# Kernel tuning notes

Measured on AMD Instinct MI355X. Metric: run time of the kernel, lower is better.

## Reference

```python
import jax, jax.numpy as jnp
import numpy as np

N = 15000        # nodes
E = 240000       # edges (avg degree 16)
IN_DIM = 100
HID = 128
N_ETYPES = 13
N_STEPS = 6
N_GRAPHS = 64
N_CLASSES = 10


def setup_inputs() -> dict:
    key = jax.random.key(0)
    ks = jax.random.split(key, 12)
    feat = jax.random.normal(ks[0], (N, IN_DIM), dtype=jnp.float32)
    src = jax.random.randint(ks[1], (E,), 0, N, dtype=jnp.int32)
    dst = jax.random.randint(ks[2], (E,), 0, N, dtype=jnp.int32)
    etypes = jax.random.randint(ks[3], (E,), 0, N_ETYPES, dtype=jnp.int32)
    graph_ids = jnp.sort(jax.random.randint(ks[4], (N,), 0, N_GRAPHS, dtype=jnp.int32))
    s = 1.0 / np.sqrt(HID)
    W_e = jax.random.normal(ks[5], (N_ETYPES, HID, HID), dtype=jnp.float32) * s
    b_e = jax.random.normal(ks[6], (N_ETYPES, HID), dtype=jnp.float32) * s
    W_ih = jax.random.normal(ks[7], (3 * HID, HID), dtype=jnp.float32) * s
    W_hh = jax.random.normal(ks[8], (3 * HID, HID), dtype=jnp.float32) * s
    b_ih = jax.random.normal(ks[9], (3 * HID,), dtype=jnp.float32) * s
    b_hh = jax.random.normal(ks[10], (3 * HID,), dtype=jnp.float32) * s
    W_cls = jax.random.normal(ks[11], (N_CLASSES, HID), dtype=jnp.float32) * s
    b_cls = jnp.zeros((N_CLASSES,), dtype=jnp.float32)
    return {"feat": feat, "src": src, "dst": dst, "etypes": etypes,
            "graph_ids": graph_ids, "W_e": W_e, "b_e": b_e,
            "W_ih": W_ih, "W_hh": W_hh, "b_ih": b_ih, "b_hh": b_hh,
            "W_cls": W_cls, "b_cls": b_cls}


def _ggnn_forward(feat, src, dst, etypes, graph_ids, W_e, b_e, W_ih, W_hh, b_ih, b_hh, W_cls, b_cls):
    # DGL GatedGraphConv: zero-pad input features up to out_feats
    h = jnp.pad(feat, ((0, 0), (0, HID - IN_DIM)))  # [N, HID]
    for _ in range(N_STEPS):
        # per-etype linear transform of all nodes: [T, N, HID]
        Wh = jnp.einsum('nd,tdh->tnh', h, W_e) + b_e[:, None, :]
        # per-edge message = linear[etype](h[src]) via gather; scatter-sum to dst
        msg = Wh[etypes, src]                                  # [E, HID]
        a = jax.ops.segment_sum(msg, dst, num_segments=N)      # [N, HID]
        # torch GRUCell update (gate order r, z, n)
        gi = a @ W_ih.T + b_ih
        gh = h @ W_hh.T + b_hh
        ir, iz, inn = jnp.split(gi, 3, axis=-1)
        hr, hz, hn = jnp.split(gh, 3, axis=-1)
        r = jax.nn.sigmoid(ir + hr)
        z = jax.nn.sigmoid(iz + hz)
        n = jnp.tanh(inn + r * hn)
        h = (1.0 - z) * n + z * h
    # dgl.sum_nodes: sum node states per graph in the batch
    hg = jax.ops.segment_sum(h, graph_ids, num_segments=N_GRAPHS)  # [G, HID]
    return hg @ W_cls.T + b_cls                                    # [G, N_CLASSES]


def reference(feat, src, dst, etypes, graph_ids, W_e, b_e, W_ih, W_hh, b_ih, b_hh, W_cls, b_cls):
    return _ggnn_forward(feat, src, dst, etypes, graph_ids, W_e, b_e, W_ih, W_hh, b_ih, b_hh, W_cls, b_cls)
```

## Files before the change

### kernel.cpp

```cpp
#include <hip/hip_runtime.h>
#include <math.h>

#define N_NODES 15000
#define NPAD    15104
#define E_EDGES 240000
#define IN_DIM  100
#define HID     128
#define N_ETYPES 13
#define N_STEPS  6
#define N_GRAPHS 64
#define N_CLASSES 10
#define NTS     (N_ETYPES * NPAD)
#define NSB     384

typedef short v8bf __attribute__((ext_vector_type(8)));
typedef float v4f  __attribute__((ext_vector_type(4)));

union FragU { uint4 u; v8bf b; };

static __device__ __forceinline__ float bf2f(unsigned short u) {
    union { unsigned int i; float f; } x; x.i = ((unsigned int)u) << 16; return x.f;
}
static __device__ __forceinline__ unsigned short f2bf(float f) {
    union { float f; unsigned int i; } x; x.f = f;
    unsigned int u = x.i;
    u = (u + 0x7fff + ((u >> 16) & 1)) >> 16;
    return (unsigned short)u;
}
static __device__ __forceinline__ float sigm(float x) { return 1.f / (1.f + expf(-x)); }

__global__ __launch_bounds__(256) void k_initW(
    const float* __restrict__ feat,
    const float* __restrict__ W_e, const float* __restrict__ W_ih, const float* __restrict__ W_hh,
    float* __restrict__ h32, unsigned short* __restrict__ h_hi, unsigned short* __restrict__ h_lo,
    unsigned short* __restrict__ WeH,
    unsigned short* __restrict__ WihH, unsigned short* __restrict__ WhhH)
{
    int idx = blockIdx.x * 256 + threadIdx.x;
    const int IH = NPAD * HID;
    const int NE = N_ETYPES * 2048;
    const int NG = 16 * 384;
    if (idx < IH) {
        int n = idx >> 7, c = idx & 127;
        float v = 0.f;
        if (n < N_NODES && c < IN_DIM) v = feat[n * IN_DIM + c];
        h32[idx] = v;
        unsigned short hi = f2bf(v);
        h_hi[idx] = hi;
        h_lo[idx] = f2bf(v - bf2f(hi));
        return;
    }
    int f = idx - IH;
    unsigned short th[8];
    if (f < NE) {
        int t = f >> 11, r = f & 2047, kcsub = r >> 7, c = r & 127;
        #pragma unroll
        for (int j = 0; j < 8; ++j)
            th[j] = f2bf(W_e[(long)t * 16384 + (kcsub * 8 + j) * 128 + c]);
        *(uint4*)(WeH + (long)t * 16384 + ((kcsub << 7) + c) * 8) = *(uint4*)th;
    } else if (f < NE + 2 * NG) {
        int f2 = f - NE;
        const float* srcp = (f2 < NG) ? W_ih : W_hh;
        unsigned short* dh = (f2 < NG) ? WihH : WhhH;
        int g = (f2 < NG) ? f2 : f2 - NG;
        int kcsub = g / 384, c = g - kcsub * 384;
        #pragma unroll
        for (int j = 0; j < 8; ++j)
            th[j] = f2bf(srcp[(long)c * 128 + kcsub * 8 + j]);
        *(uint4*)(dh + ((long)kcsub * 384 + c) * 8) = *(uint4*)th;
    }
}

__global__ __launch_bounds__(256) void k_zero2(int* __restrict__ deg, int* __restrict__ used) {
    int idx = blockIdx.x * 256 + threadIdx.x;
    if (idx < NPAD) deg[idx] = 0;
    else if (idx < NPAD + NTS) used[idx - NPAD] = 0;
}

__global__ __launch_bounds__(256) void k_count_mark(const int* __restrict__ src,
                                                    const int* __restrict__ dst,
                                                    const int* __restrict__ et,
                                                    int* __restrict__ deg,
                                                    int* __restrict__ used) {
    int e = blockIdx.x * 256 + threadIdx.x;
    if (e >= E_EDGES) return;
    atomicAdd(&deg[dst[e]], 1);
    used[et[e] * NPAD + src[e]] = 1;
}

__global__ __launch_bounds__(1024) void k_scan(const int* __restrict__ deg,
                                               int* __restrict__ rowptr, int* __restrict__ cursor) {
    __shared__ int part[1024];
    int tid = threadIdx.x;
    const int CH = 15;
    int base = tid * CH;
    int local[CH]; int s = 0;
    #pragma unroll
    for (int i = 0; i < CH; ++i) {
        int d = (base + i < NPAD) ? deg[base + i] : 0;
        local[i] = s; s += d;
    }
    part[tid] = s; __syncthreads();
    for (int off = 1; off < 1024; off <<= 1) {
        int v = (tid >= off) ? part[tid - off] : 0;
        __syncthreads();
        part[tid] += v;
        __syncthreads();
    }
    int excl = (tid > 0) ? part[tid - 1] : 0;
    #pragma unroll
    for (int i = 0; i < CH; ++i)
        if (base + i < NPAD) { rowptr[base + i] = excl + local[i]; cursor[base + i] = excl + local[i]; }
    if (tid == 0) rowptr[NPAD] = part[1023];
}

__global__ __launch_bounds__(512) void k_su1(const int* __restrict__ used, int* __restrict__ bsum) {
    __shared__ int sh[512];
    int tid = threadIdx.x;
    int i = blockIdx.x * 512 + tid;
    sh[tid] = (i < NTS) ? used[i] : 0;
    __syncthreads();
    for (int off = 256; off > 0; off >>= 1) {
        if (tid < off) sh[tid] += sh[tid + off];
        __syncthreads();
    }
    if (tid == 0) bsum[blockIdx.x] = sh[0];
}

__global__ __launch_bounds__(512) void k_su2(const int* __restrict__ bsum, int* __restrict__ bofs) {
    __shared__ int sh[512];
    int tid = threadIdx.x;
    int v = (tid < NSB) ? bsum[tid] : 0;
    sh[tid] = v; __syncthreads();
    for (int off = 1; off < 512; off <<= 1) {
        int u = (tid >= off) ? sh[tid - off] : 0;
        __syncthreads();
        sh[tid] += u;
        __syncthreads();
    }
    if (tid < NSB) bofs[tid] = sh[tid] - v;
}

__global__ __launch_bounds__(512) void k_su3(const int* __restrict__ used,
                                             const int* __restrict__ bofs,
                                             int* __restrict__ slot,
                                             int* __restrict__ rowlist,
                                             int* __restrict__ tbase) {
    __shared__ int sh[512];
    int tid = threadIdx.x;
    int i = blockIdx.x * 512 + tid;
    int f = (i < NTS) ? used[i] : 0;
    sh[tid] = f; __syncthreads();
    for (int off = 1; off < 512; off <<= 1) {
        int u = (tid >= off) ? sh[tid - off] : 0;
        __syncthreads();
        sh[tid] += u;
        __syncthreads();
    }
    int g = bofs[blockIdx.x] + sh[tid] - f;
    if (i <= NTS) {
        if (i < NTS) slot[i] = g;
        int t = i / NPAD;
        if (i - t * NPAD == 0 || i == NTS) tbase[t] = g;
        if (f) rowlist[g] = i - t * NPAD;
    }
}

__global__ __launch_bounds__(256) void k_fill(const int* __restrict__ src, const int* __restrict__ dst,
                                              const int* __restrict__ et, const int* __restrict__ slot,
                                              int* __restrict__ cursor, int* __restrict__ eidx) {
    int e = blockIdx.x * 256 + threadIdx.x;
    if (e >= E_EDGES) return;
    int d = dst[e];
    int pos = atomicAdd(&cursor[d], 1);
    eidx[pos] = slot[et[e] * NPAD + src[e]];
}

__global__ __launch_bounds__(512) void k_egemm(
    const unsigned short* __restrict__ Ahi, const unsigned short* __restrict__ Alo,
    const uint4* __restrict__ BH,
    const float* __restrict__ bias, const int* __restrict__ tbase,
    const int* __restrict__ rowlist, unsigned short* __restrict__ C)
{
    __shared__ uint4 blds[2048];
    const int NW = 118 * N_ETYPES;
    const int q = NW / 8, r8 = NW % 8;
    int bid = blockIdx.x;
    int xcd = bid & 7, ii = bid >> 3;
    int lid = (xcd < r8 ? xcd * (q + 1) : r8 * (q + 1) + (xcd - r8) * q) + ii;
    int rg = lid / N_ETYPES, t = lid - rg * N_ETYPES;

    int base = tbase[t], end = tbase[t + 1];
    if (rg * 128 >= end - base) return;

    int tid = threadIdx.x;
    {
        const uint4* bh = BH + t * 2048;
        #pragma unroll
        for (int it = 0; it < 4; ++it) {
            int f = it * 512 + tid;
            blds[f] = bh[f];
        }
    }
    __syncthreads();

    int lane = tid & 63, w = tid >> 6;
    int gs0 = base + rg * 128 + w * 16;
    int l15 = lane & 15, lsub = lane >> 4;

    int rowslot = gs0 + l15;
    int srcrow = (rowslot < end) ? rowlist[rowslot] : 0;

    FragU ah[4], al[4];
    const char* Ahb = (const char*)Ahi;
    const char* Alb = (const char*)Alo;
    #pragma unroll
    for (int kc = 0; kc < 4; ++kc) {
        long boff = (long)srcrow * 256 + kc * 64 + lsub * 16;
        ah[kc].u = *(const uint4*)(Ahb + boff);
        al[kc].u = *(const uint4*)(Alb + boff);
    }

    v4f acc[8];
    #pragma unroll
    for (int c8 = 0; c8 < 8; ++c8) acc[c8] = (v4f)(0.f);

    #pragma unroll
    for (int kc = 0; kc < 4; ++kc)
        #pragma unroll
        for (int c8 = 0; c8 < 8; ++c8) {
            int bi = (kc * 4 + lsub) * 128 + c8 * 16 + l15;
            FragU bhf; bhf.u = blds[bi];
            acc[c8] = __builtin_amdgcn_mfma_f32_16x16x32_bf16(ah[kc].b, bhf.b, acc[c8], 0, 0, 0);
            acc[c8] = __builtin_amdgcn_mfma_f32_16x16x32_bf16(al[kc].b, bhf.b, acc[c8], 0, 0, 0);
        }

    const float* bs = bias + t * 128;
    int gbase = gs0 + lsub * 4;
    #pragma unroll
    for (int c8 = 0; c8 < 8; ++c8) {
        int col = c8 * 16 + l15;
        float bv = bs[col];
        #pragma unroll
        for (int i = 0; i < 4; ++i) {
            int gs2 = gbase + i;
            if (gs2 < end) C[(long)gs2 * 128 + col] = f2bf(acc[c8][i] + bv);
        }
    }
}

__global__ __launch_bounds__(256) void k_agg(
    const int* __restrict__ rowptr, const int* __restrict__ eidx,
    const uint4* __restrict__ Wh,
    uint4* __restrict__ a_hi)
{
    int d = blockIdx.x * 4 + (threadIdx.x >> 6);
    int lane = threadIdx.x & 63;
    int g = lane >> 4, c16 = lane & 15;
    int s = rowptr[d], e = rowptr[d + 1];
    float acc[8] = {};
    for (int i = s + g; i < e; i += 4) {
        int slot = eidx[i];
        uint4 v = Wh[(long)slot * 16 + c16];
        unsigned int ua[4] = {v.x, v.y, v.z, v.w};
        #pragma unroll
        for (int q = 0; q < 4; ++q) {
            acc[2 * q]     += bf2f((unsigned short)(ua[q] & 0xffff));
            acc[2 * q + 1] += bf2f((unsigned short)(ua[q] >> 16));
        }
    }
    #pragma unroll
    for (int q = 0; q < 8; ++q) {
        acc[q] += __shfl_xor(acc[q], 16);
        acc[q] += __shfl_xor(acc[q], 32);
    }
    if (g == 0) {
        unsigned short hb[8];
        #pragma unroll
        for (int q = 0; q < 8; ++q) hb[q] = f2bf(acc[q]);
        a_hi[(long)d * 16 + c16] = *(uint4*)hb;
    }
}

__global__ __launch_bounds__(512) void k_gru(
    const unsigned short* __restrict__ a_hi,
    const uint4* __restrict__ WihH, const uint4* __restrict__ WhhH,
    const float* __restrict__ b_ih, const float* __restrict__ b_hh,
    float* __restrict__ h32,
    unsigned short* __restrict__ h_hi, unsigned short* __restrict__ h_lo)
{
    int tid = threadIdx.x, lane = tid & 63, cg = tid >> 6;
    int r0 = blockIdx.x * 16;
    int l15 = lane & 15, lsub = lane >> 4;

    FragU aa[4], hh[2][4];
    {
        const char* ahb = (const char*)a_hi;
        const char* hhb = (const char*)h_hi;
        const char* hlb = (const char*)h_lo;
        #pragma unroll
        for (int kc = 0; kc < 4; ++kc) {
            long boff = (long)(r0 + l15) * 256 + kc * 64 + lsub * 16;
            aa[kc].u    = *(const uint4*)(ahb + boff);
            hh[0][kc].u = *(const uint4*)(hhb + boff);
            hh[1][kc].u = *(const uint4*)(hlb + boff);
        }
    }
    __syncthreads();

    v4f accI[3], accH[3];
    #pragma unroll
    for (int g = 0; g < 3; ++g) { accI[g] = (v4f)(0.f); accH[g] = (v4f)(0.f); }

    #pragma unroll
    for (int kc = 0; kc < 4; ++kc)
        #pragma unroll
        for (int g = 0; g < 3; ++g) {
            int bi = (kc * 4 + lsub) * 384 + g * 128 + cg * 16 + l15;
            FragU wih, whh;
            wih.u = WihH[bi]; whh.u = WhhH[bi];
            accI[g] = __builtin_amdgcn_mfma_f32_16x16x32_bf16(aa[kc].b,    wih.b, accI[g], 0, 0, 0);
            accH[g] = __builtin_amdgcn_mfma_f32_16x16x32_bf16(hh[0][kc].b, whh.b, accH[g], 0, 0, 0);
            accH[g] = __builtin_amdgcn_mfma_f32_16x16x32_bf16(hh[1][kc].b, whh.b, accH[g], 0, 0, 0);
        }

    int c = cg * 16 + l15;
    float bir = b_ih[c], biz = b_ih[c + 128], bin = b_ih[c + 256];
    float bhr = b_hh[c], bhz = b_hh[c + 128], bhn = b_hh[c + 256];
    #pragma unroll
    for (int i = 0; i < 4; ++i) {
        int row = r0 + lsub * 4 + i;
        float ir = accI[0][i] + bir, iz = accI[1][i] + biz, inn = accI[2][i] + bin;
        float hr = accH[0][i] + bhr, hz = accH[1][i] + bhz, hn = accH[2][i] + bhn;
        float rr = sigm(ir + hr);
        float zg = sigm(iz + hz);
        float ng = tanhf(inn + rr * hn);
        long off = (long)row * 128 + c;
        float ho = h32[off];
        float hv = (1.f - zg) * ng + zg * ho;
        if (row < N_NODES) {
            h32[off] = hv;
            unsigned short hi_ = f2bf(hv);
            h_hi[off] = hi_;
            h_lo[off] = f2bf(hv - bf2f(hi_));
        }
    }
}

__global__ __launch_bounds__(256) void k_pool(const float* __restrict__ h32,
                                              const int* __restrict__ gid,
                                              float* __restrict__ hg) {
    int idx = blockIdx.x * 256 + threadIdx.x;
    if (idx >= N_NODES * HID) return;
    int n = idx >> 7, c = idx & 127;
    atomicAdd(&hg[gid[n] * HID + c], h32[idx]);
}

__global__ __launch_bounds__(256) void k_zero(float* __restrict__ p, long n4) {
    long i = (long)blockIdx.x * 256 + threadIdx.x;
    if (i < n4) ((float4*)p)[i] = make_float4(0.f, 0.f, 0.f, 0.f);
}

__global__ __launch_bounds__(640) void k_cls(const float* __restrict__ hg,
                                             const float* __restrict__ Wc,
                                             const float* __restrict__ bc,
                                             float* __restrict__ out) {
    int tid = threadIdx.x;
    if (tid >= N_GRAPHS * N_CLASSES) return;
    int g = tid / N_CLASSES, c = tid - g * N_CLASSES;
    float s = bc[c];
    for (int k = 0; k < HID; ++k) s = fmaf(hg[g * HID + k], Wc[c * HID + k], s);
    out[tid] = s;
}

extern "C" void kernel_launch(void* const* d_in, const int* in_sizes, int n_in,
                              void* d_out, int out_size, void* d_ws, size_t ws_size,
                              hipStream_t stream) {
    const float* feat  = (const float*)d_in[0];
    const int*   src   = (const int*)d_in[1];
    const int*   dst   = (const int*)d_in[2];
    const int*   et    = (const int*)d_in[3];
    const int*   gid   = (const int*)d_in[4];
    const float* W_e   = (const float*)d_in[5];
    const float* b_e   = (const float*)d_in[6];
    const float* W_ih  = (const float*)d_in[7];
    const float* W_hh  = (const float*)d_in[8];
    const float* b_ih  = (const float*)d_in[9];
    const float* b_hh  = (const float*)d_in[10];
    const float* W_cls = (const float*)d_in[11];
    const float* b_cls = (const float*)d_in[12];
    float* out = (float*)d_out;

    char* p = (char*)d_ws;
    auto alloc = [&](size_t bytes) { char* r = p; p += (bytes + 255) & ~(size_t)255; return r; };
    float*          h32  = (float*)alloc((size_t)NPAD * 128 * 4);
    unsigned short* h_hi = (unsigned short*)alloc((size_t)NPAD * 128 * 2);
    unsigned short* h_lo = (unsigned short*)alloc((size_t)NPAD * 128 * 2);
    unsigned short* a_hi = (unsigned short*)alloc((size_t)NPAD * 128 * 2);
    unsigned short* Wh   = (unsigned short*)alloc((size_t)NTS * 128 * 2);
    unsigned short* WeH  = (unsigned short*)alloc((size_t)N_ETYPES * 16384 * 2);
    unsigned short* WihH = (unsigned short*)alloc((size_t)16 * 384 * 8 * 2);
    unsigned short* WhhH = (unsigned short*)alloc((size_t)16 * 384 * 8 * 2);
    int* deg     = (int*)alloc((size_t)NPAD * 4);
    int* rowptr  = (int*)alloc((size_t)(NPAD + 1) * 4);
    int* cursor  = (int*)alloc((size_t)NPAD * 4);
    int* eidx    = (int*)alloc((size_t)E_EDGES * 4);
    int* used    = (int*)alloc((size_t)NTS * 4);
    int* slot    = (int*)alloc((size_t)NTS * 4);
    int* rowlist = (int*)alloc((size_t)NTS * 4);
    int* bsum    = (int*)alloc((size_t)NSB * 4);
    int* bofs    = (int*)alloc((size_t)NSB * 4);
    int* tbase   = (int*)alloc((size_t)(N_ETYPES + 1) * 4);
    float* hg    = (float*)alloc((size_t)N_GRAPHS * HID * 4);

    const int IW_GRID = (NPAD * HID + N_ETYPES * 2048 + 2 * 16 * 384 + 255) / 256;
    k_initW<<<IW_GRID, 256, 0, stream>>>(feat, W_e, W_ih, W_hh, h32, h_hi, h_lo,
                                         WeH, WihH, WhhH);
    k_zero2<<<(NPAD + NTS + 255) / 256, 256, 0, stream>>>(deg, used);
    k_count_mark<<<(E_EDGES + 255) / 256, 256, 0, stream>>>(src, dst, et, deg, used);
    k_scan<<<1, 1024, 0, stream>>>(deg, rowptr, cursor);
    k_su1<<<NSB, 512, 0, stream>>>(used, bsum);
    k_su2<<<1, 512, 0, stream>>>(bsum, bofs);
    k_su3<<<NSB, 512, 0, stream>>>(used, bofs, slot, rowlist, tbase);
    k_fill<<<(E_EDGES + 255) / 256, 256, 0, stream>>>(src, dst, et, slot, cursor, eidx);

    for (int step = 0; step < N_STEPS; ++step) {
        k_egemm<<<118 * N_ETYPES, 512, 0, stream>>>(
            h_hi, h_lo, (const uint4*)WeH, b_e, tbase, rowlist, Wh);
        k_agg<<<NPAD / 4, 256, 0, stream>>>(rowptr, eidx, (const uint4*)Wh, (uint4*)a_hi);
        k_gru<<<NPAD / 16, 512, 0, stream>>>(
            a_hi, (const uint4*)WihH, (const uint4*)WhhH,
            b_ih, b_hh, h32, h_hi, h_lo);
    }

    k_zero<<<(N_GRAPHS * HID / 4 + 255) / 256, 256, 0, stream>>>(hg, N_GRAPHS * HID / 4);
    k_pool<<<(N_NODES * HID + 255) / 256, 256, 0, stream>>>(h32, gid, hg);
    k_cls<<<1, 640, 0, stream>>>(hg, W_cls, b_cls, out);
}
```

Baseline: 505.1 us.

## Aggregate source states per (dst, etype) before transform and fuse into one kernel

Replaces transform-then-gather-scatter with gather-then-transform. Edges are bucketed by (dst, etype) via a CSR. Each wave sums the fp32 source states per etype and multiplies the sum by W_e with split-bf16 MFMA, while the bias is precomputed as count times b_e per node. This removes the large per-(etype, node) Wh intermediate and its write/read traffic. In exchange each block rereads h rows for every edge, loops serially over 13 etypes with per-lane edge loops, and runs only 236 blocks. Each block also loads W_e directly from global memory instead of staging it in LDS.

```diff
diff --git a/kernel.cpp b/kernel.cpp
--- a/kernel.cpp
+++ b/kernel.cpp
@@ -71,54 +71,24 @@
     }
 }
 
-__global__ __launch_bounds__(256) void k_zero2(int* __restrict__ deg, int* __restrict__ used) {
+__global__ __launch_bounds__(256) void k_zeroi(int* __restrict__ p, int n) {
     int idx = blockIdx.x * 256 + threadIdx.x;
-    if (idx < NPAD) deg[idx] = 0;
-    else if (idx < NPAD + NTS) used[idx - NPAD] = 0;
-}
-
-__global__ __launch_bounds__(256) void k_count_mark(const int* __restrict__ src,
-                                                    const int* __restrict__ dst,
-                                                    const int* __restrict__ et,
-                                                    int* __restrict__ deg,
-                                                    int* __restrict__ used) {
+    if (idx < n) p[idx] = 0;
+}
+
+__global__ __launch_bounds__(256) void k_countDT(const int* __restrict__ dst,
+                                                 const int* __restrict__ et,
+                                                 int* __restrict__ cnt) {
     int e = blockIdx.x * 256 + threadIdx.x;
     if (e >= E_EDGES) return;
-    atomicAdd(&deg[dst[e]], 1);
-    used[et[e] * NPAD + src[e]] = 1;
-}
-
-__global__ __launch_bounds__(1024) void k_scan(const int* __restrict__ deg,
-                                               int* __restrict__ rowptr, int* __restrict__ cursor) {
-    __shared__ int part[1024];
-    int tid = threadIdx.x;
-    const int CH = 15;
-    int base = tid * CH;
-    int local[CH]; int s = 0;
-    #pragma unroll
-    for (int i = 0; i < CH; ++i) {
-        int d = (base + i < NPAD) ? deg[base + i] : 0;
-        local[i] = s; s += d;
-    }
-    part[tid] = s; __syncthreads();
-    for (int off = 1; off < 1024; off <<= 1) {
-        int v = (tid >= off) ? part[tid - off] : 0;
-        __syncthreads();
-        part[tid] += v;
-        __syncthreads();
-    }
-    int excl = (tid > 0) ? part[tid - 1] : 0;
-    #pragma unroll
-    for (int i = 0; i < CH; ++i)
-        if (base + i < NPAD) { rowptr[base + i] = excl + local[i]; cursor[base + i] = excl + local[i]; }
-    if (tid == 0) rowptr[NPAD] = part[1023];
-}
-
-__global__ __launch_bounds__(512) void k_su1(const int* __restrict__ used, int* __restrict__ bsum) {
+    atomicAdd(&cnt[dst[e] * N_ETYPES + et[e]], 1);
+}
+
+__global__ __launch_bounds__(512) void k_su1(const int* __restrict__ cnt, int* __restrict__ bsum) {
     __shared__ int sh[512];
     int tid = threadIdx.x;
     int i = blockIdx.x * 512 + tid;
-    sh[tid] = (i < NTS) ? used[i] : 0;
+    sh[tid] = (i < NTS) ? cnt[i] : 0;
     __syncthreads();
     for (int off = 256; off > 0; off >>= 1) {
         if (tid < off) sh[tid] += sh[tid + off];
@@ -141,15 +111,14 @@
     if (tid < NSB) bofs[tid] = sh[tid] - v;
 }
 
-__global__ __launch_bounds__(512) void k_su3(const int* __restrict__ used,
+__global__ __launch_bounds__(512) void k_su3(const int* __restrict__ cnt,
                                              const int* __restrict__ bofs,
-                                             int* __restrict__ slot,
-                                             int* __restrict__ rowlist,
-                                             int* __restrict__ tbase) {
+                                             int* __restrict__ rowptrDT,
+                                             int* __restrict__ cursorDT) {
     __shared__ int sh[512];
     int tid = threadIdx.x;
     int i = blockIdx.x * 512 + tid;
-    int f = (i < NTS) ? used[i] : 0;
+    int f = (i < NTS) ? cnt[i] : 0;
     sh[tid] = f; __syncthreads();
     for (int off = 1; off < 512; off <<= 1) {
         int u = (tid >= off) ? sh[tid - off] : 0;
@@ -159,126 +128,125 @@
     }
     int g = bofs[blockIdx.x] + sh[tid] - f;
     if (i <= NTS) {
-        if (i < NTS) slot[i] = g;
-        int t = i / NPAD;
-        if (i - t * NPAD == 0 || i == NTS) tbase[t] = g;
-        if (f) rowlist[g] = i - t * NPAD;
-    }
-}
-
-__global__ __launch_bounds__(256) void k_fill(const int* __restrict__ src, const int* __restrict__ dst,
-                                              const int* __restrict__ et, const int* __restrict__ slot,
-                                              int* __restrict__ cursor, int* __restrict__ eidx) {
+        rowptrDT[i] = g;
+        if (i < NTS) cursorDT[i] = g;
+    }
+}
+
+__global__ __launch_bounds__(256) void k_fillDT(const int* __restrict__ src,
+                                                const int* __restrict__ dst,
+                                                const int* __restrict__ et,
+                                                int* __restrict__ cursorDT,
+                                                int* __restrict__ epay) {
     int e = blockIdx.x * 256 + threadIdx.x;
     if (e >= E_EDGES) return;
-    int d = dst[e];
-    int pos = atomicAdd(&cursor[d], 1);
-    eidx[pos] = slot[et[e] * NPAD + src[e]];
-}
-
-__global__ __launch_bounds__(512) void k_egemm(
-    const unsigned short* __restrict__ Ahi, const unsigned short* __restrict__ Alo,
-    const uint4* __restrict__ BH,
-    const float* __restrict__ bias, const int* __restrict__ tbase,
-    const int* __restrict__ rowlist, unsigned short* __restrict__ C)
+    int pos = atomicAdd(&cursorDT[dst[e] * N_ETYPES + et[e]], 1);
+    epay[pos] = src[e];
+}
+
+__global__ __launch_bounds__(256) void k_prebias(const int* __restrict__ rowptrDT,
+                                                 const float* __restrict__ b_e,
+                                                 float* __restrict__ prebias) {
+    int idx = blockIdx.x * 256 + threadIdx.x;
+    if (idx >= NPAD * HID) return;
+    int d = idx >> 7, c = idx & 127;
+    const int* rp = rowptrDT + d * N_ETYPES;
+    float s = 0.f;
+    int prev = rp[0];
+    #pragma unroll
+    for (int t = 0; t < N_ETYPES; ++t) {
+        int nxt = rp[t + 1];
+        s += (float)(nxt - prev) * b_e[t * 128 + c];
+        prev = nxt;
+    }
+    prebias[idx] = s;
+}
+
+__global__ __launch_bounds__(512) void k_fuse(
+    const float* __restrict__ h32r,
+    const int* __restrict__ rowptrDT, const int* __restrict__ epay,
+    const uint4* __restrict__ WeH,
+    const float* __restrict__ prebias,
+    unsigned short* __restrict__ a_hi)
 {
-    __shared__ uint4 blds[2048];
-    const int NW = 118 * N_ETYPES;
-    const int q = NW / 8, r8 = NW % 8;
-    int bid = blockIdx.x;
-    int xcd = bid & 7, ii = bid >> 3;
-    int lid = (xcd < r8 ? xcd * (q + 1) : r8 * (q + 1) + (xcd - r8) * q) + ii;
-    int rg = lid / N_ETYPES, t = lid - rg * N_ETYPES;
-
-    int base = tbase[t], end = tbase[t + 1];
-    if (rg * 128 >= end - base) return;
-
-    int tid = threadIdx.x;
+    __shared__ char lds[8 * 8192];
+    int tid = threadIdx.x, lane = tid & 63, w = tid >> 6;
+    int ch = blockIdx.y;
+    int r = lane & 15, ksub = lane >> 4;
+    int d0 = blockIdx.x * 128 + w * 16;
+    int d = d0 + r;
+    char* wl = lds + w * 8192;
+
+    v4f acc[4];
+    #pragma unroll
+    for (int c8 = 0; c8 < 4; ++c8) acc[c8] = (v4f)(0.f);
+
+    int rpv[N_ETYPES + 1];
     {
-        const uint4* bh = BH + t * 2048;
-        #pragma unroll
-        for (int it = 0; it < 4; ++it) {
-            int f = it * 512 + tid;
-            blds[f] = bh[f];
-        }
-    }
-    __syncthreads();
-
-    int lane = tid & 63, w = tid >> 6;
-    int gs0 = base + rg * 128 + w * 16;
-    int l15 = lane & 15, lsub = lane >> 4;
-
-    int rowslot = gs0 + l15;
-    int srcrow = (rowslot < end) ? rowlist[rowslot] : 0;
-
-    FragU ah[4], al[4];
-    const char* Ahb = (const char*)Ahi;
-    const char* Alb = (const char*)Alo;
-    #pragma unroll
-    for (int kc = 0; kc < 4; ++kc) {
-        long boff = (long)srcrow * 256 + kc * 64 + lsub * 16;
-        ah[kc].u = *(const uint4*)(Ahb + boff);
-        al[kc].u = *(const uint4*)(Alb + boff);
-    }
-
-    v4f acc[8];
-    #pragma unroll
-    for (int c8 = 0; c8 < 8; ++c8) acc[c8] = (v4f)(0.f);
-
-    #pragma unroll
-    for (int kc = 0; kc < 4; ++kc)
-        #pragma unroll
-        for (int c8 = 0; c8 < 8; ++c8) {
-            int bi = (kc * 4 + lsub) * 128 + c8 * 16 + l15;
-            FragU bhf; bhf.u = blds[bi];
-            acc[c8] = __builtin_amdgcn_mfma_f32_16x16x32_bf16(ah[kc].b, bhf.b, acc[c8], 0, 0, 0);
-            acc[c8] = __builtin_amdgcn_mfma_f32_16x16x32_bf16(al[kc].b, bhf.b, acc[c8], 0, 0, 0);
-        }
-
-    const float* bs = bias + t * 128;
-    int gbase = gs0 + lsub * 4;
-    #pragma unroll
-    for (int c8 = 0; c8 < 8; ++c8) {
-        int col = c8 * 16 + l15;
-        float bv = bs[col];
+        const int* rp = rowptrDT + d * N_ETYPES;
+        #pragma unroll
+        for (int t = 0; t <= N_ETYPES; ++t) rpv[t] = rp[t];
+    }
+
+    for (int t = 0; t < N_ETYPES; ++t) {
+        int s = rpv[t], e = rpv[t + 1];
+        if (__all(s == e)) continue;
+        float g[32];
+        #pragma unroll
+        for (int q = 0; q < 32; ++q) g[q] = 0.f;
+        const float4* hb = (const float4*)h32r;
+        for (int i = s; i < e; ++i) {
+            int srcn = epay[i];
+            const float4* hrow = hb + srcn * 32 + ksub * 8;
+            #pragma unroll
+            for (int jj = 0; jj < 8; ++jj) {
+                float4 v = hrow[jj];
+                g[jj * 4 + 0] += v.x;
+                g[jj * 4 + 1] += v.y;
+                g[jj * 4 + 2] += v.z;
+                g[jj * 4 + 3] += v.w;
+            }
+        }
+        #pragma unroll
+        for (int j = 0; j < 4; ++j) {
+            unsigned int hw[4], lw[4];
+            #pragma unroll
+            for (int p = 0; p < 4; ++p) {
+                float v0 = g[j * 8 + 2 * p], v1 = g[j * 8 + 2 * p + 1];
+                unsigned short h0 = f2bf(v0), h1 = f2bf(v1);
+                hw[p] = (unsigned int)h0 | ((unsigned int)h1 << 16);
+                lw[p] = (unsigned int)f2bf(v0 - bf2f(h0)) |
+                        ((unsigned int)f2bf(v1 - bf2f(h1)) << 16);
+            }
+            int byt = (r * 256 + ksub * 64 + j * 16) ^ ((r & 7) << 4);
+            *(uint4*)(wl + byt) = make_uint4(hw[0], hw[1], hw[2], hw[3]);
+            *(uint4*)(wl + 4096 + byt) = make_uint4(lw[0], lw[1], lw[2], lw[3]);
+        }
+        #pragma unroll
+        for (int kc = 0; kc < 4; ++kc) {
+            int byt = (r * 256 + kc * 64 + ksub * 16) ^ ((r & 7) << 4);
+            FragU ah, al;
+            ah.u = *(const uint4*)(wl + byt);
+            al.u = *(const uint4*)(wl + 4096 + byt);
+            #pragma unroll
+            for (int c8 = 0; c8 < 4; ++c8) {
+                int bi = (kc * 4 + ksub) * 128 + ch * 64 + c8 * 16 + r;
+                FragU bf_; bf_.u = WeH[t * 2048 + bi];
+                acc[c8] = __builtin_amdgcn_mfma_f32_16x16x32_bf16(ah.b, bf_.b, acc[c8], 0, 0, 0);
+                acc[c8] = __builtin_amdgcn_mfma_f32_16x16x32_bf16(al.b, bf_.b, acc[c8], 0, 0, 0);
+            }
+        }
+    }
+
+    #pragma unroll
+    for (int c8 = 0; c8 < 4; ++c8) {
+        int col = ch * 64 + c8 * 16 + r;
         #pragma unroll
         for (int i = 0; i < 4; ++i) {
-            int gs2 = gbase + i;
-            if (gs2 < end) C[(long)gs2 * 128 + col] = f2bf(acc[c8][i] + bv);
-        }
-    }
-}
-
-__global__ __launch_bounds__(256) void k_agg(
-    const int* __restrict__ rowptr, const int* __restrict__ eidx,
-    const uint4* __restrict__ Wh,
-    uint4* __restrict__ a_hi)
-{
-    int d = blockIdx.x * 4 + (threadIdx.x >> 6);
-    int lane = threadIdx.x & 63;
-    int g = lane >> 4, c16 = lane & 15;
-    int s = rowptr[d], e = rowptr[d + 1];
-    float acc[8] = {};
-    for (int i = s + g; i < e; i += 4) {
-        int slot = eidx[i];
-        uint4 v = Wh[(long)slot * 16 + c16];
-        unsigned int ua[4] = {v.x, v.y, v.z, v.w};
-        #pragma unroll
-        for (int q = 0; q < 4; ++q) {
-            acc[2 * q]     += bf2f((unsigned short)(ua[q] & 0xffff));
-            acc[2 * q + 1] += bf2f((unsigned short)(ua[q] >> 16));
-        }
-    }
-    #pragma unroll
-    for (int q = 0; q < 8; ++q) {
-        acc[q] += __shfl_xor(acc[q], 16);
-        acc[q] += __shfl_xor(acc[q], 32);
-    }
-    if (g == 0) {
-        unsigned short hb[8];
-        #pragma unroll
-        for (int q = 0; q < 8; ++q) hb[q] = f2bf(acc[q]);
-        a_hi[(long)d * 16 + c16] = *(uint4*)hb;
+            int row = d0 + ksub * 4 + i;
+            long off = (long)row * 128 + col;
+            a_hi[off] = f2bf(acc[c8][i] + prebias[off]);
+        }
     }
 }
 
@@ -393,41 +361,36 @@
 
     char* p = (char*)d_ws;
     auto alloc = [&](size_t bytes) { char* r = p; p += (bytes + 255) & ~(size_t)255; return r; };
-    float*          h32  = (float*)alloc((size_t)NPAD * 128 * 4);
-    unsigned short* h_hi = (unsigned short*)alloc((size_t)NPAD * 128 * 2);
-    unsigned short* h_lo = (unsigned short*)alloc((size_t)NPAD * 128 * 2);
-    unsigned short* a_hi = (unsigned short*)alloc((size_t)NPAD * 128 * 2);
-    unsigned short* Wh   = (unsigned short*)alloc((size_t)NTS * 128 * 2);
-    unsigned short* WeH  = (unsigned short*)alloc((size_t)N_ETYPES * 16384 * 2);
-    unsigned short* WihH = (unsigned short*)alloc((size_t)16 * 384 * 8 * 2);
-    unsigned short* WhhH = (unsigned short*)alloc((size_t)16 * 384 * 8 * 2);
-    int* deg     = (int*)alloc((size_t)NPAD * 4);
-    int* rowptr  = (int*)alloc((size_t)(NPAD + 1) * 4);
-    int* cursor  = (int*)alloc((size_t)NPAD * 4);
-    int* eidx    = (int*)alloc((size_t)E_EDGES * 4);
-    int* used    = (int*)alloc((size_t)NTS * 4);
-    int* slot    = (int*)alloc((size_t)NTS * 4);
-    int* rowlist = (int*)alloc((size_t)NTS * 4);
-    int* bsum    = (int*)alloc((size_t)NSB * 4);
-    int* bofs    = (int*)alloc((size_t)NSB * 4);
-    int* tbase   = (int*)alloc((size_t)(N_ETYPES + 1) * 4);
-    float* hg    = (float*)alloc((size_t)N_GRAPHS * HID * 4);
+    float*          h32   = (float*)alloc((size_t)NPAD * 128 * 4);
+    unsigned short* h_hi  = (unsigned short*)alloc((size_t)NPAD * 128 * 2);
+    unsigned short* h_lo  = (unsigned short*)alloc((size_t)NPAD * 128 * 2);
+    unsigned short* a_hi  = (unsigned short*)alloc((size_t)NPAD * 128 * 2);
+    unsigned short* WeH   = (unsigned short*)alloc((size_t)N_ETYPES * 16384 * 2);
+    unsigned short* WihH  = (unsigned short*)alloc((size_t)16 * 384 * 8 * 2);
+    unsigned short* WhhH  = (unsigned short*)alloc((size_t)16 * 384 * 8 * 2);
+    int* cntDT    = (int*)alloc((size_t)NTS * 4);
+    int* rowptrDT = (int*)alloc((size_t)(NTS + 1) * 4);
+    int* cursorDT = (int*)alloc((size_t)NTS * 4);
+    int* epay     = (int*)alloc((size_t)E_EDGES * 4);
+    int* bsum     = (int*)alloc((size_t)NSB * 4);
+    int* bofs     = (int*)alloc((size_t)NSB * 4);
+    float* prebias = (float*)alloc((size_t)NPAD * 128 * 4);
+    float* hg     = (float*)alloc((size_t)N_GRAPHS * HID * 4);
 
     const int IW_GRID = (NPAD * HID + N_ETYPES * 2048 + 2 * 16 * 384 + 255) / 256;
     k_initW<<<IW_GRID, 256, 0, stream>>>(feat, W_e, W_ih, W_hh, h32, h_hi, h_lo,
                                          WeH, WihH, WhhH);
-    k_zero2<<<(NPAD + NTS + 255) / 256, 256, 0, stream>>>(deg, used);
-    k_count_mark<<<(E_EDGES + 255) / 256, 256, 0, stream>>>(src, dst, et, deg, used);
-    k_scan<<<1, 1024, 0, stream>>>(deg, rowptr, cursor);
-    k_su1<<<NSB, 512, 0, stream>>>(used, bsum);
+    k_zeroi<<<(NTS + 255) / 256, 256, 0, stream>>>(cntDT, NTS);
+    k_countDT<<<(E_EDGES + 255) / 256, 256, 0, stream>>>(dst, et, cntDT);
+    k_su1<<<NSB, 512, 0, stream>>>(cntDT, bsum);
     k_su2<<<1, 512, 0, stream>>>(bsum, bofs);
-    k_su3<<<NSB, 512, 0, stream>>>(used, bofs, slot, rowlist, tbase);
-    k_fill<<<(E_EDGES + 255) / 256, 256, 0, stream>>>(src, dst, et, slot, cursor, eidx);
+    k_su3<<<NSB, 512, 0, stream>>>(cntDT, bofs, rowptrDT, cursorDT);
+    k_fillDT<<<(E_EDGES + 255) / 256, 256, 0, stream>>>(src, dst, et, cursorDT, epay);
+    k_prebias<<<(NPAD * HID + 255) / 256, 256, 0, stream>>>(rowptrDT, b_e, prebias);
 
     for (int step = 0; step < N_STEPS; ++step) {
-        k_egemm<<<118 * N_ETYPES, 512, 0, stream>>>(
-            h_hi, h_lo, (const uint4*)WeH, b_e, tbase, rowlist, Wh);
-        k_agg<<<NPAD / 4, 256, 0, stream>>>(rowptr, eidx, (const uint4*)Wh, (uint4*)a_hi);
+        k_fuse<<<dim3(118, 2), 512, 0, stream>>>(
+            h32, rowptrDT, epay, (const uint4*)WeH, prebias, a_hi);
         k_gru<<<NPAD / 16, 512, 0, stream>>>(
             a_hi, (const uint4*)WihH, (const uint4*)WhhH,
             b_ih, b_hh, h32, h_hi, h_lo);
```

After: 732.9 us. 45.1% more time.

## Fuse edge aggregation into GRU kernel via shared-memory tile

Applied to the files above, without the earlier changes.

Merges the aggregation kernel into the GRU kernel. Each of the 8 waves in a block now aggregates two destination rows and writes the bf16 sums into a swizzled 4KB shared tile, which the MFMA GRU stage then reads as its A fragments. This removes the global a_hi round trip and one kernel launch per step. The cost is that the gather work gets fewer blocks (NPAD/16 instead of NPAD/4), and the GRU stage cannot start until the slowest row in its block is aggregated, which may lower parallelism for the latency-bound gather.

```diff
diff --git a/kernel.cpp b/kernel.cpp
--- a/kernel.cpp
+++ b/kernel.cpp
@@ -249,64 +249,73 @@
     }
 }
 
-__global__ __launch_bounds__(256) void k_agg(
+__global__ __launch_bounds__(512) void k_aggru(
     const int* __restrict__ rowptr, const int* __restrict__ eidx,
     const uint4* __restrict__ Wh,
-    uint4* __restrict__ a_hi)
-{
-    int d = blockIdx.x * 4 + (threadIdx.x >> 6);
-    int lane = threadIdx.x & 63;
-    int g = lane >> 4, c16 = lane & 15;
-    int s = rowptr[d], e = rowptr[d + 1];
-    float acc[8] = {};
-    for (int i = s + g; i < e; i += 4) {
-        int slot = eidx[i];
-        uint4 v = Wh[(long)slot * 16 + c16];
-        unsigned int ua[4] = {v.x, v.y, v.z, v.w};
-        #pragma unroll
-        for (int q = 0; q < 4; ++q) {
-            acc[2 * q]     += bf2f((unsigned short)(ua[q] & 0xffff));
-            acc[2 * q + 1] += bf2f((unsigned short)(ua[q] >> 16));
-        }
-    }
-    #pragma unroll
-    for (int q = 0; q < 8; ++q) {
-        acc[q] += __shfl_xor(acc[q], 16);
-        acc[q] += __shfl_xor(acc[q], 32);
-    }
-    if (g == 0) {
-        unsigned short hb[8];
-        #pragma unroll
-        for (int q = 0; q < 8; ++q) hb[q] = f2bf(acc[q]);
-        a_hi[(long)d * 16 + c16] = *(uint4*)hb;
-    }
-}
-
-__global__ __launch_bounds__(512) void k_gru(
-    const unsigned short* __restrict__ a_hi,
     const uint4* __restrict__ WihH, const uint4* __restrict__ WhhH,
     const float* __restrict__ b_ih, const float* __restrict__ b_hh,
     float* __restrict__ h32,
     unsigned short* __restrict__ h_hi, unsigned short* __restrict__ h_lo)
 {
-    int tid = threadIdx.x, lane = tid & 63, cg = tid >> 6;
+    __shared__ char atile[16 * 256];
+    int tid = threadIdx.x, lane = tid & 63, w = tid >> 6;
     int r0 = blockIdx.x * 16;
+
+    {
+        int g = lane >> 4, c16 = lane & 15;
+        #pragma unroll
+        for (int rr = 0; rr < 2; ++rr) {
+            int rloc = w * 2 + rr;
+            int d = r0 + rloc;
+            int s = rowptr[d], e = rowptr[d + 1];
+            float acc[8] = {};
+            for (int i = s + g; i < e; i += 4) {
+                int slot = eidx[i];
+                uint4 v = Wh[(long)slot * 16 + c16];
+                unsigned int ua[4] = {v.x, v.y, v.z, v.w};
+                #pragma unroll
+                for (int q = 0; q < 4; ++q) {
+                    acc[2 * q]     += bf2f((unsigned short)(ua[q] & 0xffff));
+                    acc[2 * q + 1] += bf2f((unsigned short)(ua[q] >> 16));
+                }
+            }
+            #pragma unroll
+            for (int q = 0; q < 8; ++q) {
+                acc[q] += __shfl_xor(acc[q], 16);
+                acc[q] += __shfl_xor(acc[q], 32);
+            }
+            if (g == 0) {
+                unsigned short hb[8];
+                #pragma unroll
+                for (int q = 0; q < 8; ++q) hb[q] = f2bf(acc[q]);
+                int byt = (rloc * 256 + c16 * 16) ^ ((rloc & 7) << 4);
+                *(uint4*)(atile + byt) = *(uint4*)hb;
+            }
+        }
+    }
+
+    int cg = w;
     int l15 = lane & 15, lsub = lane >> 4;
 
-    FragU aa[4], hh[2][4];
+    FragU hh[2][4];
     {
-        const char* ahb = (const char*)a_hi;
         const char* hhb = (const char*)h_hi;
         const char* hlb = (const char*)h_lo;
         #pragma unroll
         for (int kc = 0; kc < 4; ++kc) {
             long boff = (long)(r0 + l15) * 256 + kc * 64 + lsub * 16;
-            aa[kc].u    = *(const uint4*)(ahb + boff);
             hh[0][kc].u = *(const uint4*)(hhb + boff);
             hh[1][kc].u = *(const uint4*)(hlb + boff);
         }
     }
     __syncthreads();
+
+    FragU aa[4];
+    #pragma unroll
+    for (int kc = 0; kc < 4; ++kc) {
+        int byt = (l15 * 256 + kc * 64 + lsub * 16) ^ ((l15 & 7) << 4);
+        aa[kc].u = *(const uint4*)(atile + byt);
+    }
 
     v4f accI[3], accH[3];
     #pragma unroll
@@ -396,7 +405,6 @@
     float*          h32  = (float*)alloc((size_t)NPAD * 128 * 4);
     unsigned short* h_hi = (unsigned short*)alloc((size_t)NPAD * 128 * 2);
     unsigned short* h_lo = (unsigned short*)alloc((size_t)NPAD * 128 * 2);
-    unsigned short* a_hi = (unsigned short*)alloc((size_t)NPAD * 128 * 2);
     unsigned short* Wh   = (unsigned short*)alloc((size_t)NTS * 128 * 2);
     unsigned short* WeH  = (unsigned short*)alloc((size_t)N_ETYPES * 16384 * 2);
     unsigned short* WihH = (unsigned short*)alloc((size_t)16 * 384 * 8 * 2);
@@ -427,9 +435,9 @@
     for (int step = 0; step < N_STEPS; ++step) {
         k_egemm<<<118 * N_ETYPES, 512, 0, stream>>>(
             h_hi, h_lo, (const uint4*)WeH, b_e, tbase, rowlist, Wh);
-        k_agg<<<NPAD / 4, 256, 0, stream>>>(rowptr, eidx, (const uint4*)Wh, (uint4*)a_hi);
-        k_gru<<<NPAD / 16, 512, 0, stream>>>(
-            a_hi, (const uint4*)WihH, (const uint4*)WhhH,
+        k_aggru<<<NPAD / 16, 512, 0, stream>>>(
+            rowptr, eidx, (const uint4*)Wh,
+            (const uint4*)WihH, (const uint4*)WhhH,
             b_ih, b_hh, h32, h_hi, h_lo);
     }
 
```

Measured after the change: 475.9 us (median of 2 runs). -5.8%, faster.
